# Optimization experiments

Measured on AMD Instinct MI355X. Metric: run time of the kernel, lower is better.

## Reference

```python
import jax, jax.numpy as jnp
from jax import lax
import numpy as np

H, W = 2160, 3840
KSIZE = 31


def _gaussian_kernel(size: int) -> jnp.ndarray:
    # sigma per OpenCV convention used in the module
    sigma = 0.3 * ((size - 1) * 0.5 - 1) + 0.8
    d = jnp.arange(size, dtype=jnp.float32) - (size // 2)
    k1 = jnp.exp(-(d ** 2) / (2.0 * sigma ** 2))
    k1 = k1 / k1.sum()
    k2 = jnp.outer(k1, k1)  # [k, k]
    # depthwise kernel for groups=3: [out=3, in/groups=1, k, k]
    return jnp.broadcast_to(k2[None, None], (3, 1, size, size))


def setup_inputs() -> dict:
    key = jax.random.key(0)
    k_img, = jax.random.split(key, 1)
    image = jax.random.uniform(k_img, (1, 3, H, W), dtype=jnp.float32)  # already /255-normalized
    mask = jnp.zeros((1, 1, H, W), dtype=jnp.float32)
    # two blur regions (x, y, w, h) -> mask[:, :, y:y+h, x:x+w] = 1
    mask = mask.at[:, :, 400:1400, 600:2600].set(1.0)
    mask = mask.at[:, :, 100:500, 3000:3700].set(1.0)
    kernel = _gaussian_kernel(KSIZE)
    return {"image": image, "mask": mask, "kernel": kernel}


def reference(image, mask, kernel):
    # depthwise 2D Gaussian conv, SAME padding == padding=k//2 for odd k, stride 1
    blurred = lax.conv_general_dilated(
        image, kernel,
        window_strides=(1, 1), padding="SAME",
        feature_group_count=3,
        dimension_numbers=("NCHW", "OIHW", "NCHW"),
    )
    out = image * (1.0 - mask) + blurred * mask  # mask broadcasts over channel dim
    # squeeze batch, NCHW -> HWC, back to 0..255 scale (uint8 cast omitted for float baseline)
    return out[0].transpose(1, 2, 0) * 255.0
```

## Files before the change

kernel.cpp:

```cpp
#include <hip/hip_runtime.h>

#define HH 2160
#define WW 3840
#define K 31
#define RAD 15
#define TW 64
#define TH 16
#define IW 96
#define IH 46
#define NTHREADS 256
#define NROUND 5
#define TMPW 100

#define GLDS(gp, lp) __builtin_amdgcn_global_load_lds(                         \
    (const __attribute__((address_space(1))) void*)(gp),                       \
    (__attribute__((address_space(3))) void*)(lp), 16, 0, 0)

__device__ __forceinline__ float fcomp(float4 v, int p) {
    switch (p) { case 0: return v.x; case 1: return v.y; case 2: return v.z; default: return v.w; }
}

__device__ __forceinline__ float uniformf(float x) {
    return __uint_as_float(__builtin_amdgcn_readfirstlane(__float_as_uint(x)));
}

__global__ __launch_bounds__(NTHREADS, 4) void blur_masked_kernel(
    const float* __restrict__ img, const float* __restrict__ mask,
    const float* __restrict__ kern, float* __restrict__ out)
{
    __shared__ float s_in[NROUND * NTHREADS * 4];
    __shared__ float s_tmp[TH * TMPW];
    __shared__ float s_k1[K];

    const int tilesX = WW / TW;
    const int tx = blockIdx.x % tilesX;
    const int ty = blockIdx.x / tilesX;
    const int x0 = tx * TW;
    const int y0 = ty * TH;
    const int t  = threadIdx.x;

    const int hr  = t >> 4;
    const int hc0 = (t & 15) * 4;

    if (t < K) {
        float s = 0.f;
        const float* kr = kern + t * K;
        #pragma unroll
        for (int j = 0; j < K; ++j) s += kr[j];
        s_k1[t] = s;
    }

    const size_t pix0 = (size_t)(y0 + hr) * WW + (x0 + hc0);
    float4 mv = *(const float4*)(mask + pix0);
    int anyLocal = (mv.x != 0.f) | (mv.y != 0.f) | (mv.z != 0.f) | (mv.w != 0.f);
    int any = __syncthreads_or(anyLocal);

    if (!any) {
        const size_t HW = (size_t)HH * WW;
        float4 i0 = *(const float4*)(img + pix0);
        float4 i1 = *(const float4*)(img + HW + pix0);
        float4 i2 = *(const float4*)(img + 2 * HW + pix0);
        float* ob = out + pix0 * 3;
        *(float4*)(ob)     = make_float4(i0.x * 255.f, i1.x * 255.f, i2.x * 255.f, i0.y * 255.f);
        *(float4*)(ob + 4) = make_float4(i1.y * 255.f, i2.y * 255.f, i0.z * 255.f, i1.z * 255.f);
        *(float4*)(ob + 8) = make_float4(i2.z * 255.f, i0.w * 255.f, i1.w * 255.f, i2.w * 255.f);
        return;
    }

    float k1r[K];
    #pragma unroll
    for (int j = 0; j < K; ++j) k1r[j] = uniformf(s_k1[j]);

    const bool interior = (tx >= 1) && (tx <= 58) && (ty >= 1) && (ty <= 133);

    auto stage = [&](int ch) {
        const float* imc = img + (size_t)ch * HH * WW;
        if (interior) {
            #pragma unroll
            for (int k2 = 0; k2 < NROUND; ++k2) {
                int i = t + k2 * NTHREADS;
                int r = i / (IW / 4), c4 = i % (IW / 4);
                int gy = y0 - RAD + r;
                if (gy > HH - 1) gy = HH - 1;
                const float* gp = imc + (size_t)gy * WW + (x0 - 16 + 4 * c4);
                GLDS(gp, s_in + 4 * i);
            }
        } else {
            #pragma unroll
            for (int k2 = 0; k2 < NROUND; ++k2) {
                int i = t + k2 * NTHREADS;
                int r = i / (IW / 4), c4 = i % (IW / 4);
                int gy = y0 - RAD + r, gx = x0 - 16 + 4 * c4;
                float4 v = make_float4(0.f, 0.f, 0.f, 0.f);
                if (r < IH && gy >= 0 && gy < HH && gx >= 0 && gx < WW)
                    v = *(const float4*)(imc + (size_t)gy * WW + gx);
                *(float4*)(s_in + 4 * i) = v;
            }
        }
    };

    stage(0);

    float o[12];

    #pragma unroll
    for (int ch = 0; ch < 3; ++ch) {
        __syncthreads();

        #pragma unroll
        for (int k2 = 0; k2 < 3; ++k2) {
            int i = t + k2 * NTHREADS;
            int r = i / IW, cc = i % IW;
            float a0 = 0.f, a1 = 0.f;
            #pragma unroll
            for (int u = 0; u < 39; ++u) {
                float v = s_in[(r + u) * IW + cc];
                if (u <= 30) a0 += v * k1r[u];
                if (u >= 8)  a1 += v * k1r[u - 8];
            }
            s_tmp[r * TMPW + cc]       = a0;
            s_tmp[(r + 8) * TMPW + cc] = a1;
        }
        float4 iv = *(const float4*)(s_in + (hr + RAD) * IW + hc0 + 16);

        __syncthreads();

        if (ch < 2) stage(ch + 1);

        float a0 = 0.f, a1 = 0.f, a2 = 0.f, a3 = 0.f;
        const float* rowp = s_tmp + hr * TMPW + hc0;
        #pragma unroll
        for (int q = 0; q < 9; ++q) {
            float4 w = *(const float4*)(rowp + 4 * q);
            #pragma unroll
            for (int e = 0; e < 4; ++e) {
                const int idx = 4 * q + e;
                float v = fcomp(w, e);
                if (idx - 1 >= 0 && idx - 1 <= 30) a0 += v * k1r[idx - 1];
                if (idx - 2 >= 0 && idx - 2 <= 30) a1 += v * k1r[idx - 2];
                if (idx - 3 >= 0 && idx - 3 <= 30) a2 += v * k1r[idx - 3];
                if (idx - 4 >= 0 && idx - 4 <= 30) a3 += v * k1r[idx - 4];
            }
        }

        float bl[4] = {a0, a1, a2, a3};
        #pragma unroll
        for (int p = 0; p < 4; ++p) {
            float m = fcomp(mv, p);
            o[p * 3 + ch] = (fcomp(iv, p) * (1.f - m) + bl[p] * m) * 255.f;
        }
    }

    float* ob = out + pix0 * 3;
    *(float4*)(ob)     = make_float4(o[0], o[1], o[2],  o[3]);
    *(float4*)(ob + 4) = make_float4(o[4], o[5], o[6],  o[7]);
    *(float4*)(ob + 8) = make_float4(o[8], o[9], o[10], o[11]);
}

extern "C" void kernel_launch(void* const* d_in, const int* in_sizes, int n_in,
                              void* d_out, int out_size, void* d_ws, size_t ws_size,
                              hipStream_t stream) {
    const float* img  = (const float*)d_in[0];
    const float* mask = (const float*)d_in[1];
    const float* kern = (const float*)d_in[2];
    float* out = (float*)d_out;
    int nblocks = (WW / TW) * (HH / TH);
    blur_masked_kernel<<<nblocks, NTHREADS, 0, stream>>>(img, mask, kern, out);
}
```

Before: 59.04 us.

## Compute eight vertical outputs per thread and trim staged LDS rows

The vertical pass now has 192 threads, each producing 8 consecutive rows of one column from 38 LDS loads. The old scheme used 256 threads over 3 rounds, each producing 2 rows from 39 loads. Staging is trimmed to the exact 46 input rows, which removes the padding rows and the clamp on the interior path. This is meant to cut LDS read traffic in the vertical pass, at the cost of idling 64 threads during that phase and holding more accumulators in registers.

```diff
diff --git a/kernel.cpp b/kernel.cpp
--- a/kernel.cpp
+++ b/kernel.cpp
@@ -9,7 +9,7 @@
 #define IW 96
 #define IH 46
 #define NTHREADS 256
-#define NROUND 5
+#define NF4 (IH * (IW / 4))
 #define TMPW 100
 
 #define GLDS(gp, lp) __builtin_amdgcn_global_load_lds(                         \
@@ -28,7 +28,7 @@
     const float* __restrict__ img, const float* __restrict__ mask,
     const float* __restrict__ kern, float* __restrict__ out)
 {
-    __shared__ float s_in[NROUND * NTHREADS * 4];
+    __shared__ float s_in[NF4 * 4];
     __shared__ float s_tmp[TH * TMPW];
     __shared__ float s_k1[K];
 
@@ -77,24 +77,26 @@
         const float* imc = img + (size_t)ch * HH * WW;
         if (interior) {
             #pragma unroll
-            for (int k2 = 0; k2 < NROUND; ++k2) {
+            for (int k2 = 0; k2 < 5; ++k2) {
                 int i = t + k2 * NTHREADS;
-                int r = i / (IW / 4), c4 = i % (IW / 4);
-                int gy = y0 - RAD + r;
-                if (gy > HH - 1) gy = HH - 1;
-                const float* gp = imc + (size_t)gy * WW + (x0 - 16 + 4 * c4);
-                GLDS(gp, s_in + 4 * i);
+                if (i < NF4) {
+                    int r = i / (IW / 4), c4 = i % (IW / 4);
+                    const float* gp = imc + (size_t)(y0 - RAD + r) * WW + (x0 - 16 + 4 * c4);
+                    GLDS(gp, s_in + 4 * i);
+                }
             }
         } else {
             #pragma unroll
-            for (int k2 = 0; k2 < NROUND; ++k2) {
+            for (int k2 = 0; k2 < 5; ++k2) {
                 int i = t + k2 * NTHREADS;
-                int r = i / (IW / 4), c4 = i % (IW / 4);
-                int gy = y0 - RAD + r, gx = x0 - 16 + 4 * c4;
-                float4 v = make_float4(0.f, 0.f, 0.f, 0.f);
-                if (r < IH && gy >= 0 && gy < HH && gx >= 0 && gx < WW)
-                    v = *(const float4*)(imc + (size_t)gy * WW + gx);
-                *(float4*)(s_in + 4 * i) = v;
+                if (i < NF4) {
+                    int r = i / (IW / 4), c4 = i % (IW / 4);
+                    int gy = y0 - RAD + r, gx = x0 - 16 + 4 * c4;
+                    float4 v = make_float4(0.f, 0.f, 0.f, 0.f);
+                    if (gy >= 0 && gy < HH && gx >= 0 && gx < WW)
+                        v = *(const float4*)(imc + (size_t)gy * WW + gx);
+                    *(float4*)(s_in + 4 * i) = v;
+                }
             }
         }
     };
@@ -103,23 +105,27 @@
 
     float o[12];
 
+    const int vc = t % 96;
+    const int vh = t / 96;
+
     #pragma unroll
     for (int ch = 0; ch < 3; ++ch) {
         __syncthreads();
 
-        #pragma unroll
-        for (int k2 = 0; k2 < 3; ++k2) {
-            int i = t + k2 * NTHREADS;
-            int r = i / IW, cc = i % IW;
-            float a0 = 0.f, a1 = 0.f;
+        if (vh < 2) {
+            float acc[8] = {0.f, 0.f, 0.f, 0.f, 0.f, 0.f, 0.f, 0.f};
+            const int ybase = vh * 8;
             #pragma unroll
-            for (int u = 0; u < 39; ++u) {
-                float v = s_in[(r + u) * IW + cc];
-                if (u <= 30) a0 += v * k1r[u];
-                if (u >= 8)  a1 += v * k1r[u - 8];
+            for (int s = 0; s < 38; ++s) {
+                float v = s_in[(ybase + s) * IW + vc];
+                #pragma unroll
+                for (int j = 0; j < 8; ++j) {
+                    if (s - j >= 0 && s - j <= 30) acc[j] += v * k1r[s - j];
+                }
             }
-            s_tmp[r * TMPW + cc]       = a0;
-            s_tmp[(r + 8) * TMPW + cc] = a1;
+            #pragma unroll
+            for (int j = 0; j < 8; ++j)
+                s_tmp[(ybase + j) * TMPW + vc] = acc[j];
         }
         float4 iv = *(const float4*)(s_in + (hr + RAD) * IW + hc0 + 16);
 
```

Measured after the change: 59.51 us. Within noise of the previous version (+0.8%).
